# Kernel optimization log

Hardware: AMD Instinct MI355X
Metric: run time of the kernel (lower is better)

## Reference

```python
import jax, jax.numpy as jnp
import numpy as np


def _soft_attention(h, context, W_in, W_out):
    """Luong soft-dot attention. h: [B,H], context: [B,L,H].
    W_in: [H,H] (in,out layout), W_out: [2H,H]."""
    target = h @ W_in                                  # [B, H]
    attn = jnp.einsum('blh,bh->bl', context, target)   # [B, L]
    p = jax.nn.softmax(attn, axis=-1)                  # [B, L]
    weighted_ctx = jnp.einsum('bl,blh->bh', p, context)  # [B, H]
    h_tilde = jnp.tanh(jnp.concatenate([weighted_ctx, h], axis=1) @ W_out)  # [B, H]
    return h_tilde, p


def setup_inputs() -> dict:
    key = jax.random.key(0)
    ks = jax.random.split(key, 13)
    B, L, H = 64, 512, 1024
    s2 = 1.0 / np.sqrt(2 * H)
    s1 = 1.0 / np.sqrt(H)
    return {
        'h_tilde_s': jax.random.normal(ks[0], (B, H), jnp.float32),
        'h_tilde_o': jax.random.normal(ks[1], (B, H), jnp.float32),
        'h_tilde_a': jax.random.normal(ks[2], (B, H), jnp.float32),
        'enc_out': jax.random.normal(ks[3], (B, L, H), jnp.float32),
        'full_feature_len': 36,
        'W_as': jax.random.normal(ks[4], (2 * H, H), jnp.float32) * s2,
        'W_so': jax.random.normal(ks[5], (2 * H, H), jnp.float32) * s2,
        'W_oa': jax.random.normal(ks[6], (2 * H, H), jnp.float32) * s2,
        'Win_as': jax.random.normal(ks[7], (H, H), jnp.float32) * s1,
        'Win_so': jax.random.normal(ks[8], (H, H), jnp.float32) * s1,
        'Win_oa': jax.random.normal(ks[9], (H, H), jnp.float32) * s1,
        'Wout_as': jax.random.normal(ks[10], (2 * H, H), jnp.float32) * s2,
        'Wout_so': jax.random.normal(ks[11], (2 * H, H), jnp.float32) * s2,
        'Wout_oa': jax.random.normal(ks[12], (2 * H, H), jnp.float32) * s2,
    }


def reference(h_tilde_s, h_tilde_o, h_tilde_a, enc_out, full_feature_len,
              W_as, W_so, W_oa, Win_as, Win_so, Win_oa,
              Wout_as, Wout_so, Wout_oa):
    # Relational contexts via concat + linear(no bias) + tanh
    h_as = jnp.tanh(jnp.concatenate([h_tilde_a, h_tilde_s], axis=1) @ W_as)  # [B,H]
    h_so = jnp.tanh(jnp.concatenate([h_tilde_s, h_tilde_o], axis=1) @ W_so)
    h_oa = jnp.tanh(jnp.concatenate([h_tilde_o, h_tilde_a], axis=1) @ W_oa)
    # Three parallel soft-dot attentions over encoder output
    sa_as, _ = _soft_attention(h_as, enc_out, Win_as, Wout_as)
    sa_so, _ = _soft_attention(h_so, enc_out, Win_so, Wout_so)
    sa_oa, _ = _soft_attention(h_oa, enc_out, Win_oa, Wout_oa)
    B, H = sa_as.shape
    F = full_feature_len
    # repeat_interleave of size-1 dim == broadcast tile to [B, F, H]
    ctx_mas = jnp.broadcast_to(sa_as[:, None, :], (B, F, H))
    ctx_mso = jnp.broadcast_to(sa_so[:, None, :], (B, F, H))
    ctx_moa = jnp.broadcast_to(sa_oa[:, None, :], (B, F, H))
    return (ctx_mas, ctx_mso, ctx_moa)
```

## Files before the change

kernel.cpp:

```cpp
#include <hip/hip_runtime.h>

constexpr int BB = 64;
constexpr int LL = 512;
constexpr int HH = 1024;
constexpr int SPLITS = 16;

struct Ptr3 { const float* p[3]; };

template<int K0, int K1>
__global__ __launch_bounds__(256)
void gemm_skinny(Ptr3 A0, Ptr3 A1, Ptr3 Wp, float* __restrict__ part)
{
    constexpr int K = K0 + K1;
    constexpr int KRANGE = K / SPLITS;
    __shared__ float As[32][64];
    __shared__ float Ws[32][64];
    const int r   = blockIdx.z;
    const int n0  = blockIdx.x * 64;
    const int ks  = blockIdx.y * KRANGE;
    const int tid = threadIdx.x;
    const float* a0 = A0.p[r];
    const float* a1 = A1.p[r];
    const float* w  = Wp.p[r];

    const int tn = tid & 15;
    const int tm = tid >> 4;

    float acc[4][4] = {};

    for (int kt = ks; kt < ks + KRANGE; kt += 32) {
        {
            const int m   = tid >> 2;
            const int kk0 = (tid & 3) << 3;
            const int kg  = kt + kk0;
            const float* src = (K1 == 0 || kg < K0) ? (a0 + (size_t)m * HH + kg)
                                                    : (a1 + (size_t)m * HH + (kg - K0));
            float4 v0 = *(const float4*)(src);
            float4 v1 = *(const float4*)(src + 4);
            As[kk0 + 0][m] = v0.x; As[kk0 + 1][m] = v0.y;
            As[kk0 + 2][m] = v0.z; As[kk0 + 3][m] = v0.w;
            As[kk0 + 4][m] = v1.x; As[kk0 + 5][m] = v1.y;
            As[kk0 + 6][m] = v1.z; As[kk0 + 7][m] = v1.w;
        }
        {
            const int j4 = (tid & 15) << 2;
            int kk = tid >> 4;
            #pragma unroll
            for (int i = 0; i < 2; i++, kk += 16) {
                *(float4*)&Ws[kk][j4] = *(const float4*)(w + (size_t)(kt + kk) * HH + n0 + j4);
            }
        }
        __syncthreads();
        #pragma unroll
        for (int kk = 0; kk < 32; kk++) {
            float4 a4 = *(const float4*)&As[kk][tm << 2];
            float4 b4 = *(const float4*)&Ws[kk][tn << 2];
            float av[4] = {a4.x, a4.y, a4.z, a4.w};
            float bv[4] = {b4.x, b4.y, b4.z, b4.w};
            #pragma unroll
            for (int i = 0; i < 4; i++)
                #pragma unroll
                for (int j = 0; j < 4; j++)
                    acc[i][j] += av[i] * bv[j];
        }
        __syncthreads();
    }

    float* dst = part + (size_t)((r * SPLITS + blockIdx.y) * 64) * HH + n0 + (tn << 2);
    #pragma unroll
    for (int i = 0; i < 4; i++) {
        const int m = (tm << 2) + i;
        *(float4*)(dst + (size_t)m * HH) = make_float4(acc[i][0], acc[i][1], acc[i][2], acc[i][3]);
    }
}

template<bool TANH>
__global__ __launch_bounds__(256)
void reduce_split(const float* __restrict__ part, float* __restrict__ dst)
{
    const int i4   = blockIdx.x * 256 + threadIdx.x;
    const int flat = i4 << 2;
    const int r    = flat >> 16;
    const int mn   = flat & 65535;
    const float* p = part + (size_t)r * SPLITS * 65536 + mn;
    float4 s = *(const float4*)p;
    #pragma unroll
    for (int y = 1; y < SPLITS; y++) {
        float4 q = *(const float4*)(p + (size_t)y * 65536);
        s.x += q.x; s.y += q.y; s.z += q.z; s.w += q.w;
    }
    if (TANH) {
        s.x = tanhf(s.x); s.y = tanhf(s.y); s.z = tanhf(s.z); s.w = tanhf(s.w);
    }
    *(float4*)(dst + (size_t)r * 65536 + mn) = s;
}

__global__ __launch_bounds__(256)
void flash_chunk(const float* __restrict__ enc, const float* __restrict__ tt,
                 float* __restrict__ opm, float* __restrict__ ms)
{
    __shared__ float o_l[4][3][HH];
    __shared__ float ms_sh[4][3][2];
    const int b    = blockIdx.x >> 5;
    const int lc   = blockIdx.x & 31;
    const int tid  = threadIdx.x;
    const int lane = tid & 63;
    const int w    = tid >> 6;

    float4 tr[3][4];
    #pragma unroll
    for (int r = 0; r < 3; r++)
        #pragma unroll
        for (int v = 0; v < 4; v++)
            tr[r][v] = *(const float4*)&tt[(size_t)(r * BB + b) * HH + (lane << 2) + (v << 8)];

    const int l0 = (lc << 4) + (w << 2);
    const float* e = enc + ((size_t)b * LL + l0) * HH + (lane << 2);
    float4 ev[4][4];
    #pragma unroll
    for (int j = 0; j < 4; j++)
        #pragma unroll
        for (int v = 0; v < 4; v++)
            ev[j][v] = *(const float4*)(e + (size_t)j * HH + (v << 8));

    float s[3][4];
    #pragma unroll
    for (int j = 0; j < 4; j++) {
        float d0 = 0.f, d1 = 0.f, d2 = 0.f;
        #pragma unroll
        for (int v = 0; v < 4; v++) {
            const float4 x = ev[j][v];
            d0 += x.x * tr[0][v].x + x.y * tr[0][v].y + x.z * tr[0][v].z + x.w * tr[0][v].w;
            d1 += x.x * tr[1][v].x + x.y * tr[1][v].y + x.z * tr[1][v].z + x.w * tr[1][v].w;
            d2 += x.x * tr[2][v].x + x.y * tr[2][v].y + x.z * tr[2][v].z + x.w * tr[2][v].w;
        }
        #pragma unroll
        for (int off = 32; off > 0; off >>= 1) {
            d0 += __shfl_xor(d0, off);
            d1 += __shfl_xor(d1, off);
            d2 += __shfl_xor(d2, off);
        }
        s[0][j] = d0; s[1][j] = d1; s[2][j] = d2;
    }

    #pragma unroll
    for (int r = 0; r < 3; r++) {
        const float m = fmaxf(fmaxf(s[r][0], s[r][1]), fmaxf(s[r][2], s[r][3]));
        float p[4];
        float sum = 0.f;
        #pragma unroll
        for (int j = 0; j < 4; j++) { p[j] = __expf(s[r][j] - m); sum += p[j]; }
        #pragma unroll
        for (int v = 0; v < 4; v++) {
            float4 o = make_float4(0.f, 0.f, 0.f, 0.f);
            #pragma unroll
            for (int j = 0; j < 4; j++) {
                const float4 x = ev[j][v];
                o.x += p[j] * x.x; o.y += p[j] * x.y;
                o.z += p[j] * x.z; o.w += p[j] * x.w;
            }
            *(float4*)&o_l[w][r][(lane << 2) + (v << 8)] = o;
        }
        if (lane == 0) { ms_sh[w][r][0] = m; ms_sh[w][r][1] = sum; }
    }
    __syncthreads();

    const int chunk = (b << 5) + lc;
    #pragma unroll
    for (int r = 0; r < 3; r++) {
        float m0 = ms_sh[0][r][0], m1 = ms_sh[1][r][0];
        float m2 = ms_sh[2][r][0], m3 = ms_sh[3][r][0];
        const float M = fmaxf(fmaxf(m0, m1), fmaxf(m2, m3));
        const float w0 = __expf(m0 - M), w1 = __expf(m1 - M);
        const float w2 = __expf(m2 - M), w3 = __expf(m3 - M);
        float4 q0 = *(const float4*)&o_l[0][r][tid << 2];
        float4 q1 = *(const float4*)&o_l[1][r][tid << 2];
        float4 q2 = *(const float4*)&o_l[2][r][tid << 2];
        float4 q3 = *(const float4*)&o_l[3][r][tid << 2];
        float4 acc;
        acc.x = w0 * q0.x + w1 * q1.x + w2 * q2.x + w3 * q3.x;
        acc.y = w0 * q0.y + w1 * q1.y + w2 * q2.y + w3 * q3.y;
        acc.z = w0 * q0.z + w1 * q1.z + w2 * q2.z + w3 * q3.z;
        acc.w = w0 * q0.w + w1 * q1.w + w2 * q2.w + w3 * q3.w;
        *(float4*)&opm[((size_t)chunk * 3 + r) * HH + (tid << 2)] = acc;
        if (tid == 0) {
            const float S = w0 * ms_sh[0][r][1] + w1 * ms_sh[1][r][1]
                          + w2 * ms_sh[2][r][1] + w3 * ms_sh[3][r][1];
            ms[((size_t)chunk * 3 + r) * 2 + 0] = M;
            ms[((size_t)chunk * 3 + r) * 2 + 1] = S;
        }
    }
}

__global__ __launch_bounds__(256)
void flash_combine(const float* __restrict__ opm, const float* __restrict__ ms,
                   float* __restrict__ wc)
{
    __shared__ float ms_l[32][2];
    const int b   = blockIdx.x;
    const int r   = blockIdx.y;
    const int tid = threadIdx.x;

    if (tid < 32) {
        const int chunk = (b << 5) + tid;
        ms_l[tid][0] = ms[((size_t)chunk * 3 + r) * 2 + 0];
        ms_l[tid][1] = ms[((size_t)chunk * 3 + r) * 2 + 1];
    }
    __syncthreads();

    float M = -3.4e38f;
    #pragma unroll 8
    for (int c = 0; c < 32; c++) M = fmaxf(M, ms_l[c][0]);

    float S = 0.f;
    float4 acc = make_float4(0.f, 0.f, 0.f, 0.f);
    #pragma unroll 4
    for (int c = 0; c < 32; c++) {
        const float wgt = __expf(ms_l[c][0] - M);
        S += wgt * ms_l[c][1];
        const int chunk = (b << 5) + c;
        float4 q = *(const float4*)&opm[((size_t)chunk * 3 + r) * HH + (tid << 2)];
        acc.x += wgt * q.x; acc.y += wgt * q.y;
        acc.z += wgt * q.z; acc.w += wgt * q.w;
    }
    const float inv = 1.0f / S;
    acc.x *= inv; acc.y *= inv; acc.z *= inv; acc.w *= inv;
    *(float4*)&wc[(size_t)(r * BB + b) * HH + (tid << 2)] = acc;
}

__global__ __launch_bounds__(256)
void reduce_tanh_broadcast(const float* __restrict__ part, const int* __restrict__ Fp,
                           float* __restrict__ out)
{
    const int i4   = blockIdx.x * 256 + threadIdx.x;
    const int flat = i4 << 2;
    const int r    = flat >> 16;
    const int mn   = flat & 65535;
    const float* p = part + (size_t)r * SPLITS * 65536 + mn;
    float4 s = *(const float4*)p;
    #pragma unroll
    for (int y = 1; y < SPLITS; y++) {
        float4 q = *(const float4*)(p + (size_t)y * 65536);
        s.x += q.x; s.y += q.y; s.z += q.z; s.w += q.w;
    }
    s.x = tanhf(s.x); s.y = tanhf(s.y); s.z = tanhf(s.z); s.w = tanhf(s.w);

    const int F  = *Fp;
    const int bb = mn >> 10;
    const int hh = mn & 1023;
    float* o = out + ((size_t)(r * BB + bb) * F) * HH + hh;
    for (int f = 0; f < F; f++)
        *(float4*)(o + (size_t)f * HH) = s;
}

extern "C" void kernel_launch(void* const* d_in, const int* in_sizes, int n_in,
                              void* d_out, int out_size, void* d_ws, size_t ws_size,
                              hipStream_t stream)
{
    (void)in_sizes; (void)n_in; (void)out_size; (void)ws_size;
    const float* hs  = (const float*)d_in[0];
    const float* ho  = (const float*)d_in[1];
    const float* ha  = (const float*)d_in[2];
    const float* enc = (const float*)d_in[3];
    const int*   Fp  = (const int*)d_in[4];
    const float* W_as    = (const float*)d_in[5];
    const float* W_so    = (const float*)d_in[6];
    const float* W_oa    = (const float*)d_in[7];
    const float* Win_as  = (const float*)d_in[8];
    const float* Win_so  = (const float*)d_in[9];
    const float* Win_oa  = (const float*)d_in[10];
    const float* Wout_as = (const float*)d_in[11];
    const float* Wout_so = (const float*)d_in[12];
    const float* Wout_oa = (const float*)d_in[13];

    float* ws   = (float*)d_ws;
    float* part = ws;
    float* hx   = ws + 3145728;
    float* tt   = ws + 3342336;
    float* wc   = ws + 3538944;
    float* opm  = ws + 3735552;
    float* msb  = ws + 10027008;

    {
        Ptr3 A0{{ha, hs, ho}};
        Ptr3 A1{{hs, ho, ha}};
        Ptr3 W {{W_as, W_so, W_oa}};
        gemm_skinny<1024, 1024><<<dim3(16, SPLITS, 3), 256, 0, stream>>>(A0, A1, W, part);
    }
    reduce_split<true><<<192, 256, 0, stream>>>(part, hx);

    {
        Ptr3 A0{{hx, hx + 65536, hx + 131072}};
        Ptr3 A1{{nullptr, nullptr, nullptr}};
        Ptr3 W {{Win_as, Win_so, Win_oa}};
        gemm_skinny<1024, 0><<<dim3(16, SPLITS, 3), 256, 0, stream>>>(A0, A1, W, part);
    }
    reduce_split<false><<<192, 256, 0, stream>>>(part, tt);

    flash_chunk<<<2048, 256, 0, stream>>>(enc, tt, opm, msb);
    flash_combine<<<dim3(64, 3), 256, 0, stream>>>(opm, msb, wc);

    {
        Ptr3 A0{{wc, wc + 65536, wc + 131072}};
        Ptr3 A1{{hx, hx + 65536, hx + 131072}};
        Ptr3 W {{Wout_as, Wout_so, Wout_oa}};
        gemm_skinny<1024, 1024><<<dim3(16, SPLITS, 3), 256, 0, stream>>>(A0, A1, W, part);
    }

    reduce_tanh_broadcast<<<192, 256, 0, stream>>>(part, Fp, (float*)d_out);
}
```

Measured before the change: 323.4 us.

## Process four L-tiles per flash block with online softmax and nontemporal output stores

Each flash_chunk block now loops over 64 encoder rows instead of 16, keeping a running max, sum and output per wave with online-softmax rescaling. This cuts the grid from 2048 to 512 blocks and shrinks the partial-output buffer and the combine work by a factor of four. The broadcast output kernel now writes with nontemporal stores so the large replicated output does not pollute the cache. The trade-off is less parallelism, fewer outstanding loads per block, and a serial dependence across loop iterations.

```diff
diff --git a/kernel.cpp b/kernel.cpp
--- a/kernel.cpp
+++ b/kernel.cpp
@@ -4,6 +4,8 @@
 constexpr int LL = 512;
 constexpr int HH = 1024;
 constexpr int SPLITS = 16;
+
+typedef float nt_float4 __attribute__((ext_vector_type(4)));
 
 struct Ptr3 { const float* p[3]; };
 
@@ -101,8 +103,8 @@
 {
     __shared__ float o_l[4][3][HH];
     __shared__ float ms_sh[4][3][2];
-    const int b    = blockIdx.x >> 5;
-    const int lc   = blockIdx.x & 31;
+    const int b    = blockIdx.x >> 3;
+    const int lc   = blockIdx.x & 7;
     const int tid  = threadIdx.x;
     const int lane = tid & 63;
     const int w    = tid >> 6;
@@ -114,62 +116,86 @@
         for (int v = 0; v < 4; v++)
             tr[r][v] = *(const float4*)&tt[(size_t)(r * BB + b) * HH + (lane << 2) + (v << 8)];
 
-    const int l0 = (lc << 4) + (w << 2);
-    const float* e = enc + ((size_t)b * LL + l0) * HH + (lane << 2);
-    float4 ev[4][4];
-    #pragma unroll
-    for (int j = 0; j < 4; j++)
+    float  m_run[3] = {-3.0e38f, -3.0e38f, -3.0e38f};
+    float  S_run[3] = {0.f, 0.f, 0.f};
+    float4 o_run[3][4];
+    #pragma unroll
+    for (int r = 0; r < 3; r++)
         #pragma unroll
         for (int v = 0; v < 4; v++)
-            ev[j][v] = *(const float4*)(e + (size_t)j * HH + (v << 8));
-
-    float s[3][4];
-    #pragma unroll
-    for (int j = 0; j < 4; j++) {
-        float d0 = 0.f, d1 = 0.f, d2 = 0.f;
-        #pragma unroll
-        for (int v = 0; v < 4; v++) {
-            const float4 x = ev[j][v];
-            d0 += x.x * tr[0][v].x + x.y * tr[0][v].y + x.z * tr[0][v].z + x.w * tr[0][v].w;
-            d1 += x.x * tr[1][v].x + x.y * tr[1][v].y + x.z * tr[1][v].z + x.w * tr[1][v].w;
-            d2 += x.x * tr[2][v].x + x.y * tr[2][v].y + x.z * tr[2][v].z + x.w * tr[2][v].w;
-        }
-        #pragma unroll
-        for (int off = 32; off > 0; off >>= 1) {
-            d0 += __shfl_xor(d0, off);
-            d1 += __shfl_xor(d1, off);
-            d2 += __shfl_xor(d2, off);
-        }
-        s[0][j] = d0; s[1][j] = d1; s[2][j] = d2;
+            o_run[r][v] = make_float4(0.f, 0.f, 0.f, 0.f);
+
+    const float* ebase = enc + ((size_t)b * LL + (lc << 6) + (w << 2)) * HH + (lane << 2);
+
+    for (int it = 0; it < 4; it++) {
+        const float* e = ebase + (size_t)(it << 4) * HH;
+        float4 ev[4][4];
+        #pragma unroll
+        for (int j = 0; j < 4; j++)
+            #pragma unroll
+            for (int v = 0; v < 4; v++)
+                ev[j][v] = *(const float4*)(e + (size_t)j * HH + (v << 8));
+
+        float s[3][4];
+        #pragma unroll
+        for (int j = 0; j < 4; j++) {
+            float d0 = 0.f, d1 = 0.f, d2 = 0.f;
+            #pragma unroll
+            for (int v = 0; v < 4; v++) {
+                const float4 x = ev[j][v];
+                d0 += x.x * tr[0][v].x + x.y * tr[0][v].y + x.z * tr[0][v].z + x.w * tr[0][v].w;
+                d1 += x.x * tr[1][v].x + x.y * tr[1][v].y + x.z * tr[1][v].z + x.w * tr[1][v].w;
+                d2 += x.x * tr[2][v].x + x.y * tr[2][v].y + x.z * tr[2][v].z + x.w * tr[2][v].w;
+            }
+            #pragma unroll
+            for (int off = 32; off > 0; off >>= 1) {
+                d0 += __shfl_xor(d0, off);
+                d1 += __shfl_xor(d1, off);
+                d2 += __shfl_xor(d2, off);
+            }
+            s[0][j] = d0; s[1][j] = d1; s[2][j] = d2;
+        }
+
+        #pragma unroll
+        for (int r = 0; r < 3; r++) {
+            const float mb = fmaxf(fmaxf(s[r][0], s[r][1]), fmaxf(s[r][2], s[r][3]));
+            const float mn_ = fmaxf(m_run[r], mb);
+            const float alpha = __expf(m_run[r] - mn_);
+            m_run[r] = mn_;
+            float p[4];
+            float psum = 0.f;
+            #pragma unroll
+            for (int j = 0; j < 4; j++) { p[j] = __expf(s[r][j] - mn_); psum += p[j]; }
+            S_run[r] = S_run[r] * alpha + psum;
+            #pragma unroll
+            for (int v = 0; v < 4; v++) {
+                float4 o = o_run[r][v];
+                o.x *= alpha; o.y *= alpha; o.z *= alpha; o.w *= alpha;
+                #pragma unroll
+                for (int j = 0; j < 4; j++) {
+                    const float4 x = ev[j][v];
+                    o.x += p[j] * x.x; o.y += p[j] * x.y;
+                    o.z += p[j] * x.z; o.w += p[j] * x.w;
+                }
+                o_run[r][v] = o;
+            }
+        }
     }
 
     #pragma unroll
     for (int r = 0; r < 3; r++) {
-        const float m = fmaxf(fmaxf(s[r][0], s[r][1]), fmaxf(s[r][2], s[r][3]));
-        float p[4];
-        float sum = 0.f;
-        #pragma unroll
-        for (int j = 0; j < 4; j++) { p[j] = __expf(s[r][j] - m); sum += p[j]; }
-        #pragma unroll
-        for (int v = 0; v < 4; v++) {
-            float4 o = make_float4(0.f, 0.f, 0.f, 0.f);
-            #pragma unroll
-            for (int j = 0; j < 4; j++) {
-                const float4 x = ev[j][v];
-                o.x += p[j] * x.x; o.y += p[j] * x.y;
-                o.z += p[j] * x.z; o.w += p[j] * x.w;
-            }
-            *(float4*)&o_l[w][r][(lane << 2) + (v << 8)] = o;
-        }
-        if (lane == 0) { ms_sh[w][r][0] = m; ms_sh[w][r][1] = sum; }
+        #pragma unroll
+        for (int v = 0; v < 4; v++)
+            *(float4*)&o_l[w][r][(lane << 2) + (v << 8)] = o_run[r][v];
+        if (lane == 0) { ms_sh[w][r][0] = m_run[r]; ms_sh[w][r][1] = S_run[r]; }
     }
     __syncthreads();
 
-    const int chunk = (b << 5) + lc;
+    const int chunk = (b << 3) + lc;
     #pragma unroll
     for (int r = 0; r < 3; r++) {
-        float m0 = ms_sh[0][r][0], m1 = ms_sh[1][r][0];
-        float m2 = ms_sh[2][r][0], m3 = ms_sh[3][r][0];
+        const float m0 = ms_sh[0][r][0], m1 = ms_sh[1][r][0];
+        const float m2 = ms_sh[2][r][0], m3 = ms_sh[3][r][0];
         const float M = fmaxf(fmaxf(m0, m1), fmaxf(m2, m3));
         const float w0 = __expf(m0 - M), w1 = __expf(m1 - M);
         const float w2 = __expf(m2 - M), w3 = __expf(m3 - M);
@@ -196,29 +222,29 @@
 void flash_combine(const float* __restrict__ opm, const float* __restrict__ ms,
                    float* __restrict__ wc)
 {
-    __shared__ float ms_l[32][2];
+    __shared__ float ms_l[8][2];
     const int b   = blockIdx.x;
     const int r   = blockIdx.y;
     const int tid = threadIdx.x;
 
-    if (tid < 32) {
-        const int chunk = (b << 5) + tid;
+    if (tid < 8) {
+        const int chunk = (b << 3) + tid;
         ms_l[tid][0] = ms[((size_t)chunk * 3 + r) * 2 + 0];
         ms_l[tid][1] = ms[((size_t)chunk * 3 + r) * 2 + 1];
     }
     __syncthreads();
 
-    float M = -3.4e38f;
-    #pragma unroll 8
-    for (int c = 0; c < 32; c++) M = fmaxf(M, ms_l[c][0]);
+    float M = -3.0e38f;
+    #pragma unroll
+    for (int c = 0; c < 8; c++) M = fmaxf(M, ms_l[c][0]);
 
     float S = 0.f;
     float4 acc = make_float4(0.f, 0.f, 0.f, 0.f);
-    #pragma unroll 4
-    for (int c = 0; c < 32; c++) {
+    #pragma unroll
+    for (int c = 0; c < 8; c++) {
         const float wgt = __expf(ms_l[c][0] - M);
         S += wgt * ms_l[c][1];
-        const int chunk = (b << 5) + c;
+        const int chunk = (b << 3) + c;
         float4 q = *(const float4*)&opm[((size_t)chunk * 3 + r) * HH + (tid << 2)];
         acc.x += wgt * q.x; acc.y += wgt * q.y;
         acc.z += wgt * q.z; acc.w += wgt * q.w;
@@ -245,12 +271,15 @@
     }
     s.x = tanhf(s.x); s.y = tanhf(s.y); s.z = tanhf(s.z); s.w = tanhf(s.w);
 
+    nt_float4 sv;
+    sv.x = s.x; sv.y = s.y; sv.z = s.z; sv.w = s.w;
+
     const int F  = *Fp;
     const int bb = mn >> 10;
     const int hh = mn & 1023;
     float* o = out + ((size_t)(r * BB + bb) * F) * HH + hh;
     for (int f = 0; f < F; f++)
-        *(float4*)(o + (size_t)f * HH) = s;
+        __builtin_nontemporal_store(sv, (nt_float4*)(o + (size_t)f * HH));
 }
 
 extern "C" void kernel_launch(void* const* d_in, const int* in_sizes, int n_in,
@@ -279,7 +308,7 @@
     float* tt   = ws + 3342336;
     float* wc   = ws + 3538944;
     float* opm  = ws + 3735552;
-    float* msb  = ws + 10027008;
+    float* msb  = ws + 5308416;
 
     {
         Ptr3 A0{{ha, hs, ho}};
@@ -297,7 +326,7 @@
     }
     reduce_split<false><<<192, 256, 0, stream>>>(part, tt);
 
-    flash_chunk<<<2048, 256, 0, stream>>>(enc, tt, opm, msb);
+    flash_chunk<<<512, 256, 0, stream>>>(enc, tt, opm, msb);
     flash_combine<<<dim3(64, 3), 256, 0, stream>>>(opm, msb, wc);
 
     {
```

After: 310.8 us. -3.9%, faster.
